# Kernel optimization log

Measured on AMD Instinct MI355X. Metric: run time of the kernel, lower is better.

The kernel has to match this reference:

```python
import jax, jax.numpy as jnp
import numpy as np

B, S, H = 1, 2048, 2048
E, I = 16, 1408
I_SHARED = 5632
TOP_K = 2


def setup_inputs() -> dict:
    key = jax.random.key(0)
    ks = jax.random.split(key, 8)
    scale = 0.02
    return {
        "hidden_states": jax.random.normal(ks[0], (B, S, H), dtype=jnp.float32),
        "router_w": jax.random.normal(ks[1], (H, E), dtype=jnp.float32) * scale,
        "expert_gate_up_w": jax.random.normal(ks[2], (E, H, 2 * I), dtype=jnp.float32) * scale,
        "expert_out_w": jax.random.normal(ks[3], (E, I, H), dtype=jnp.float32) * scale,
        "shared_ffw_gate_w": jax.random.normal(ks[4], (H, I_SHARED), dtype=jnp.float32) * scale,
        "shared_ffw_inter_w": jax.random.normal(ks[5], (H, I_SHARED), dtype=jnp.float32) * scale,
        "shared_ffw_out_w": jax.random.normal(ks[6], (I_SHARED, H), dtype=jnp.float32) * scale,
        "shared_gate_w": jax.random.normal(ks[7], (H, 1), dtype=jnp.float32) * scale,
        "top_k": TOP_K,
    }


def reference(hidden_states, router_w, expert_gate_up_w, expert_out_w,
              shared_ffw_gate_w, shared_ffw_inter_w, shared_ffw_out_w,
              shared_gate_w, top_k):
    b, s, h = hidden_states.shape
    e = router_w.shape[-1]
    x = hidden_states.reshape(-1, h)  # [T, H]

    # --- Router: softmax over experts, top-k, renormalize (norm_top_k_prob=True) ---
    router_logits = x @ router_w                        # [T, E]
    router_probs = jax.nn.softmax(router_logits, -1)
    top_p, top_i = jax.lax.top_k(router_probs, top_k)   # [T, K]
    top_p = top_p / jnp.sum(top_p, axis=-1, keepdims=True)
    # dense routing matrix [E, T] (matches one_hot-sum-transpose in source)
    one_hot = jax.nn.one_hot(top_i, e, dtype=top_p.dtype)  # [T, K, E]
    routing_full = jnp.sum(one_hot * top_p[..., None], axis=1).T  # [E, T]

    # --- Dense per-expert SwiGLU over ALL tokens (as in QwenMoeExperts) ---
    gate_up = jnp.einsum('th,ehm->etm', x, expert_gate_up_w)  # [E, T, 2I]
    gate, up = jnp.split(gate_up, 2, axis=-1)
    hidden = up * jax.nn.silu(gate)                           # [E, T, I]
    expert_out = jnp.einsum('eti,eih->eth', hidden, expert_out_w)  # [E, T, H]
    expert_contribution = jnp.einsum('eth,et->th', expert_out, routing_full)

    # --- Shared expert (SwiGLU MLP) with sigmoid gate ---
    sgate = jax.nn.silu(x @ shared_ffw_gate_w)
    sinter = x @ shared_ffw_inter_w
    shared_out = (sinter * sgate) @ shared_ffw_out_w          # [T, H]
    shared_out = shared_out * jax.nn.sigmoid(x @ shared_gate_w)

    out = (expert_contribution + shared_out).reshape(b, s, h)
    return out, router_logits
```

## Files before the change

kernel.cpp:

```cpp
#include <hip/hip_runtime.h>
#include <math.h>

typedef __attribute__((ext_vector_type(4))) float f32x4;
typedef __attribute__((ext_vector_type(2))) unsigned int u32x2;
typedef __attribute__((ext_vector_type(4))) unsigned int u32x4;
typedef __attribute__((ext_vector_type(8))) unsigned short u16x8;
typedef __attribute__((ext_vector_type(8))) __bf16 bf16x8;
typedef unsigned short ushort_t;

#define H_DIM 2048
#define T_TOK 2048
#define NEXP 16
#define I_DIM 1408
#define I2_DIM 2816
#define IS_DIM 5632
#define MAXROWS 6144

static __device__ __forceinline__ unsigned short f2bf(float f){
  union { float f; unsigned u; } v; v.f = f;
  unsigned r = v.u + 0x7FFFu + ((v.u >> 16) & 1u);
  return (unsigned short)(r >> 16);
}
static __device__ __forceinline__ float bf2f(unsigned short h){
  union { unsigned u; float f; } v; v.u = ((unsigned)h) << 16;
  return v.f;
}
static __device__ __forceinline__ float silu_f(float x){ return x / (1.f + __expf(-x)); }

static __device__ __forceinline__ void gld16(const ushort_t* g, ushort_t* l){
  __builtin_amdgcn_global_load_lds(
      (const __attribute__((address_space(1))) unsigned int*)g,
      (__attribute__((address_space(3))) unsigned int*)l, 16, 0, 0);
}

static __device__ __forceinline__ bf16x8 dsr128(unsigned byte_off){
  u32x4 r;
  asm volatile("ds_read_b128 %0, %1" : "=v"(r) : "v"(byte_off));
  return __builtin_bit_cast(bf16x8, r);
}

static __device__ __forceinline__ void tr_tile(const float* __restrict__ in,
                                               ushort_t* __restrict__ out,
                                               int K, int N, int k0, int n0){
  __shared__ float tl[128][65];
  int t = threadIdx.x;
  int lr = t >> 4;
  int lc = t & 15;
  #pragma unroll
  for (int p = 0; p < 8; p++){
    int row = p * 16 + lr;
    f32x4 v = *(const f32x4*)&in[(long)(k0 + row) * N + n0 + lc * 4];
    tl[row][lc*4 + 0] = v[0]; tl[row][lc*4 + 1] = v[1];
    tl[row][lc*4 + 2] = v[2]; tl[row][lc*4 + 3] = v[3];
  }
  __syncthreads();
  #pragma unroll
  for (int p = 0; p < 4; p++){
    int n = p * 16 + lr;
    int kc = lc * 8;
    union { ushort_t s[8]; u32x4 v; } pk;
    #pragma unroll
    for (int j = 0; j < 8; j++) pk.s[j] = f2bf(tl[kc + j][n]);
    *(u32x4*)&out[(long)(n0 + n) * K + k0 + kc] = pk.v;
  }
}

#define TR_O1 11264
#define TR_O2 16896
#define TR_O3 18304
#define TR_O4 19712
#define TR_TOT 21120

__global__ void transpose_all_k(const float* __restrict__ wgu, const float* __restrict__ wout,
                                const float* __restrict__ wsg, const float* __restrict__ wsi,
                                const float* __restrict__ wso,
                                ushort_t* __restrict__ wgu_t, ushort_t* __restrict__ wout_t,
                                ushort_t* __restrict__ wsg_t, ushort_t* __restrict__ wsi_t,
                                ushort_t* __restrict__ wso_t){
  int b = blockIdx.x;
  if (b < TR_O1){
    int e = b / 704, r = b % 704;
    int ky = r / 44, nx = r % 44;
    long zo = (long)e * H_DIM * I2_DIM;
    tr_tile(wgu + zo, wgu_t + zo, H_DIM, I2_DIM, ky * 128, nx * 64);
  } else if (b < TR_O2){
    int r = b - TR_O1;
    int e = r / 352; r %= 352;
    int ky = r / 32, nx = r % 32;
    long zo = (long)e * I_DIM * H_DIM;
    tr_tile(wout + zo, wout_t + zo, I_DIM, H_DIM, ky * 128, nx * 64);
  } else if (b < TR_O3){
    int r = b - TR_O2;
    int ky = r / 88, nx = r % 88;
    tr_tile(wsg, wsg_t, H_DIM, IS_DIM, ky * 128, nx * 64);
  } else if (b < TR_O4){
    int r = b - TR_O3;
    int ky = r / 88, nx = r % 88;
    tr_tile(wsi, wsi_t, H_DIM, IS_DIM, ky * 128, nx * 64);
  } else {
    int r = b - TR_O4;
    int ky = r / 32, nx = r % 32;
    tr_tile(wso, wso_t, IS_DIM, H_DIM, ky * 128, nx * 64);
  }
}

__global__ void router_k(const float* __restrict__ x, const float* __restrict__ rw,
                         const float* __restrict__ sgw, float* __restrict__ logits,
                         int* __restrict__ counts, int* __restrict__ lists,
                         float* __restrict__ probs, float* __restrict__ sgmul,
                         ushort_t* __restrict__ xb){
  int wid = threadIdx.x >> 6, lane = threadIdx.x & 63;
  int t = blockIdx.x * 4 + wid;
  const float* xr = x + (long)t * H_DIM;
  ushort_t* xbr = xb + (long)t * H_DIM;
  float acc[17];
  #pragma unroll
  for (int e = 0; e < 17; e++) acc[e] = 0.f;
  for (int h0 = lane * 4; h0 < H_DIM; h0 += 256){
    f32x4 xv = *(const f32x4*)&xr[h0];
    u32x2 pk;
    pk[0] = (unsigned)f2bf(xv[0]) | ((unsigned)f2bf(xv[1]) << 16);
    pk[1] = (unsigned)f2bf(xv[2]) | ((unsigned)f2bf(xv[3]) << 16);
    *(u32x2*)&xbr[h0] = pk;
    #pragma unroll
    for (int i = 0; i < 4; i++){
      float xs = xv[i];
      const float* wrow = rw + (long)(h0 + i) * NEXP;
      #pragma unroll
      for (int e = 0; e < 16; e++) acc[e] += xs * wrow[e];
      acc[16] += xs * sgw[h0 + i];
    }
  }
  #pragma unroll
  for (int e = 0; e < 17; e++)
    for (int off = 32; off >= 1; off >>= 1)
      acc[e] += __shfl_xor(acc[e], off);
  if (lane == 0){
    float* lo = logits + (long)t * NEXP;
    #pragma unroll
    for (int e = 0; e < 16; e++) lo[e] = acc[e];
    int e0 = 0;
    #pragma unroll
    for (int e = 1; e < 16; e++) if (acc[e] > acc[e0]) e0 = e;
    int e1 = (e0 == 0) ? 1 : 0;
    #pragma unroll
    for (int e = 0; e < 16; e++) if (e != e0 && acc[e] > acc[e1]) e1 = e;
    float d = acc[e1] - acc[e0];
    float ed = __expf(d);
    float p0 = 1.f / (1.f + ed);
    float p1 = ed / (1.f + ed);
    int pos0 = atomicAdd(&counts[e0], 1);
    lists[e0 * T_TOK + pos0] = t; probs[e0 * T_TOK + pos0] = p0;
    int pos1 = atomicAdd(&counts[e1], 1);
    lists[e1 * T_TOK + pos1] = t; probs[e1 * T_TOK + pos1] = p1;
    sgmul[t] = 1.f / (1.f + __expf(-acc[16]));
  }
}

__global__ void bases_k(const int* __restrict__ counts, int* __restrict__ bases){
  if (threadIdx.x == 0){
    int r = 0;
    for (int e = 0; e < NEXP; e++){ bases[e] = r; r += (counts[e] + 127) & ~127; }
  }
}

__global__ void swiglu_expert_k(const ushort_t* __restrict__ gu, ushort_t* __restrict__ hid){
  long qd = (long)blockIdx.x * 256 + threadIdx.x;
  long r = qd / (I_DIM / 8); int ic = (int)(qd % (I_DIM / 8)) * 8;
  const ushort_t* g = gu + r * I2_DIM + ic;
  u16x8 gv = *(const u16x8*)g;
  u16x8 uv = *(const u16x8*)(g + I_DIM);
  u16x8 ov;
  #pragma unroll
  for (int i = 0; i < 8; i++)
    ov[i] = f2bf(bf2f(uv[i]) * silu_f(bf2f(gv[i])));
  *(u16x8*)&hid[r * I_DIM + ic] = ov;
}

__global__ void swiglu_flat_k(ushort_t* __restrict__ sg, const ushort_t* __restrict__ si){
  long i = ((long)blockIdx.x * 256 + threadIdx.x) * 8;
  u16x8 g = *(const u16x8*)&sg[i];
  u16x8 s = *(const u16x8*)&si[i];
  u16x8 o;
  #pragma unroll
  for (int j = 0; j < 8; j++)
    o[j] = f2bf(bf2f(s[j]) * silu_f(bf2f(g[j])));
  *(u16x8*)&sg[i] = o;
}

template<int MODE>
static __device__ __forceinline__ void gemm3_body(
    const ushort_t* __restrict__ A, const ushort_t* __restrict__ Bt,
    const ushort_t* __restrict__ Bt2, ushort_t* __restrict__ Cb,
    int K, int lda, int ldbt, int ldc, int mb,
    const int* __restrict__ counts, const int* __restrict__ bases,
    const int* __restrict__ lists, const float* __restrict__ probs,
    const float* __restrict__ svec, float* __restrict__ outp, long bstride){
  int z = blockIdx.z;
  int cnt = T_TOK;
  const ushort_t* Ab = A;
  const ushort_t* Bb = Bt;
  long rbase = 0;
  if constexpr (MODE == 0){ if (z){ Bb = Bt2; Cb += (long)T_TOK * ldc; } }
  if constexpr (MODE == 1){ cnt = counts[z]; rbase = bases[z]; Bb += (long)z * bstride; }
  if constexpr (MODE == 2){ cnt = counts[z]; Ab += (long)bases[z] * lda; Bb += (long)z * bstride; }

  int kb = K / gridDim.y;
  int kbase = blockIdx.y * kb;
  Ab += kbase;
  Bb += kbase;

  int nwg = gridDim.x;
  int wgo = blockIdx.x;
  int q = nwg >> 3, r = nwg & 7;
  int xcd = wgo & 7, idx = wgo >> 3;
  int wg = (xcd < r ? xcd * (q + 1) : r * (q + 1) + (xcd - r) * q) + idx;
  int m0 = (wg % mb) * 128;
  if (m0 >= cnt) return;
  int n0 = (wg / mb) * 128;

  __shared__ ushort_t lds[3 * 8192];
  unsigned lbase = (unsigned)(size_t)(__attribute__((address_space(3))) ushort_t*)lds;

  int tid = threadIdx.x;
  int lane = tid & 63;
  int wv = tid >> 6;
  int wm = wv >> 1;
  int wn = wv & 1;

  int srow = lane >> 2;
  int sslot = ((lane & 3) ^ (srow & 3)) * 8;
  long aoff[2], boff[2];
  #pragma unroll
  for (int c = 0; c < 2; c++){
    int mr = wv * 32 + c * 16 + srow;
    int grow;
    if constexpr (MODE == 1){
      int j = m0 + mr; if (j >= cnt) j = cnt - 1;
      grow = lists[z * T_TOK + j];
    } else {
      grow = m0 + mr;
    }
    aoff[c] = (long)grow * lda + sslot;
    boff[c] = (long)(n0 + mr) * ldbt + sslot;
  }

  auto stage = [&](int t, int buf){
    long ko = (long)t * 32;
    ushort_t* dA = lds + buf * 8192 + wv * 1024;
    ushort_t* dB = dA + 4096;
    gld16(Ab + aoff[0] + ko, dA);
    gld16(Ab + aoff[1] + ko, dA + 512);
    gld16(Bb + boff[0] + ko, dB);
    gld16(Bb + boff[1] + ko, dB + 512);
  };

  f32x4 zero = {0.f, 0.f, 0.f, 0.f};
  f32x4 acc[4][4];
  #pragma unroll
  for (int i = 0; i < 4; i++)
    #pragma unroll
    for (int j = 0; j < 4; j++) acc[i][j] = zero;

  int fr = lane & 15;
  int kg = lane >> 4;
  unsigned ps = (unsigned)((kg ^ (fr & 3)) << 4);
  unsigned aoffb = (unsigned)((wm * 64 + fr) * 64) + ps;
  unsigned boffb = 8192u + (unsigned)((wn * 64 + fr) * 64) + ps;

  int nt = kb >> 5;
  stage(0, 0);
  __builtin_amdgcn_sched_barrier(0);
  stage(1, 1);

  int rb = 0, sb = 2;
  for (int t = 0; t < nt; t++){
    if (t + 2 < nt) asm volatile("s_waitcnt vmcnt(4)" ::: "memory");
    else            asm volatile("s_waitcnt vmcnt(0)" ::: "memory");
    __builtin_amdgcn_s_barrier();
    __builtin_amdgcn_sched_barrier(0);
    unsigned bufb = lbase + (unsigned)rb * 16384u;
    bf16x8 af[4], bg[4];
    #pragma unroll
    for (int f = 0; f < 4; f++){
      af[f] = dsr128(bufb + aoffb + f * 1024u);
      bg[f] = dsr128(bufb + boffb + f * 1024u);
    }
    __builtin_amdgcn_sched_barrier(0);
    if (t + 2 < nt) stage(t + 2, sb);
    asm volatile("s_waitcnt lgkmcnt(0)" ::: "memory");
    __builtin_amdgcn_sched_barrier(0);
    #pragma unroll
    for (int fm = 0; fm < 4; fm++)
      #pragma unroll
      for (int fn = 0; fn < 4; fn++)
        acc[fm][fn] = __builtin_amdgcn_mfma_f32_16x16x32_bf16(af[fm], bg[fn], acc[fm][fn], 0, 0, 0);
    rb = (rb == 2) ? 0 : rb + 1;
    sb = (sb == 2) ? 0 : sb + 1;
  }

  int colb = n0 + wn * 64 + (lane & 15);
  int rowb = m0 + wm * 64 + (lane >> 4) * 4;
  #pragma unroll
  for (int fm = 0; fm < 4; fm++){
    #pragma unroll
    for (int fn = 0; fn < 4; fn++){
      f32x4 v = acc[fm][fn];
      int col = colb + fn * 16;
      #pragma unroll
      for (int rr = 0; rr < 4; rr++){
        int m = rowb + fm * 16 + rr;
        if constexpr (MODE == 0){
          Cb[(long)m * ldc + col] = f2bf(v[rr]);
        } else if constexpr (MODE == 1){
          if (m < cnt) Cb[(rbase + m) * (long)ldc + col] = f2bf(v[rr]);
        } else if constexpr (MODE == 2){
          if (m < cnt){
            int tok = lists[z * T_TOK + m];
            float pp = probs[z * T_TOK + m];
            atomicAdd(outp + (long)tok * ldc + col, pp * v[rr]);
          }
        } else {
          atomicAdd(outp + (long)m * ldc + col, svec[m] * v[rr]);
        }
      }
    }
  }
}

#define GEMM_ARGS const ushort_t* A, const ushort_t* Bt, const ushort_t* Bt2, ushort_t* Cb, \
    int K, int lda, int ldbt, int ldc, int mb, const int* counts, const int* bases, \
    const int* lists, const float* probs, const float* svec, float* outp, long bstride
#define GEMM_PASS A, Bt, Bt2, Cb, K, lda, ldbt, ldc, mb, counts, bases, lists, probs, svec, outp, bstride

__global__ __launch_bounds__(256) void g_shared_gi(GEMM_ARGS){ gemm3_body<0>(GEMM_PASS); }
__global__ __launch_bounds__(256) void g_shared_out(GEMM_ARGS){ gemm3_body<3>(GEMM_PASS); }
__global__ __launch_bounds__(256) void g_expert_gu(GEMM_ARGS){ gemm3_body<1>(GEMM_PASS); }
__global__ __launch_bounds__(256) void g_expert_out(GEMM_ARGS){ gemm3_body<2>(GEMM_PASS); }

extern "C" void kernel_launch(void* const* d_in, const int* in_sizes, int n_in,
                              void* d_out, int out_size, void* d_ws, size_t ws_size,
                              hipStream_t stream){
  const float* x    = (const float*)d_in[0];
  const float* rw   = (const float*)d_in[1];
  const float* wgu  = (const float*)d_in[2];
  const float* wout = (const float*)d_in[3];
  const float* wsg  = (const float*)d_in[4];
  const float* wsi  = (const float*)d_in[5];
  const float* wso  = (const float*)d_in[6];
  const float* sgw  = (const float*)d_in[7];

  float* out = (float*)d_out;
  float* logits = out + (size_t)T_TOK * H_DIM;

  char* w = (char*)d_ws;
  auto alloc = [&](size_t b){ char* p = w; w += (b + 255) & ~(size_t)255; return p; };
  ushort_t* xb     = (ushort_t*)alloc((size_t)T_TOK * H_DIM * 2);
  ushort_t* wgu_t  = (ushort_t*)alloc((size_t)NEXP * I2_DIM * H_DIM * 2);
  ushort_t* wout_t = (ushort_t*)alloc((size_t)NEXP * H_DIM * I_DIM * 2);
  ushort_t* wsg_t  = (ushort_t*)alloc((size_t)IS_DIM * H_DIM * 2);
  ushort_t* wsi_t  = (ushort_t*)alloc((size_t)IS_DIM * H_DIM * 2);
  ushort_t* wso_t  = (ushort_t*)alloc((size_t)H_DIM * IS_DIM * 2);
  ushort_t* sgr    = (ushort_t*)alloc((size_t)2 * T_TOK * IS_DIM * 2);
  ushort_t* sir    = sgr + (size_t)T_TOK * IS_DIM;
  ushort_t* gu     = (ushort_t*)alloc((size_t)MAXROWS * I2_DIM * 2);
  ushort_t* hid    = (ushort_t*)alloc((size_t)MAXROWS * I_DIM * 2);
  int*   counts = (int*)alloc(64);
  int*   bases  = (int*)alloc(64);
  int*   lists  = (int*)alloc((size_t)NEXP * T_TOK * 4);
  float* probs  = (float*)alloc((size_t)NEXP * T_TOK * 4);
  float* sgmul  = (float*)alloc((size_t)T_TOK * 4);

  hipMemsetAsync(counts, 0, 64, stream);
  hipMemsetAsync(out, 0, (size_t)T_TOK * H_DIM * sizeof(float), stream);

  transpose_all_k<<<TR_TOT, 256, 0, stream>>>(wgu, wout, wsg, wsi, wso,
                                              wgu_t, wout_t, wsg_t, wsi_t, wso_t);
  router_k<<<512, 256, 0, stream>>>(x, rw, sgw, logits, counts, lists, probs, sgmul, xb);
  bases_k<<<1, 64, 0, stream>>>(counts, bases);

  g_shared_gi<<<dim3((T_TOK/128) * (IS_DIM/128), 1, 2), 256, 0, stream>>>(
      xb, wsg_t, wsi_t, sgr, H_DIM, H_DIM, H_DIM, IS_DIM, T_TOK/128,
      nullptr, nullptr, nullptr, nullptr, nullptr, nullptr, 0);
  swiglu_flat_k<<<(T_TOK * (IS_DIM/8)) / 256, 256, 0, stream>>>(sgr, sir);
  g_shared_out<<<dim3((T_TOK/128) * (H_DIM/128), 4, 1), 256, 0, stream>>>(
      sgr, wso_t, nullptr, nullptr, IS_DIM, IS_DIM, IS_DIM, H_DIM, T_TOK/128,
      nullptr, nullptr, nullptr, nullptr, sgmul, out, 0);

  g_expert_gu<<<dim3((T_TOK/128) * (I2_DIM/128), 1, NEXP), 256, 0, stream>>>(
      xb, wgu_t, nullptr, gu, H_DIM, H_DIM, H_DIM, I2_DIM, T_TOK/128,
      counts, bases, lists, probs, nullptr, nullptr, (long)I2_DIM * H_DIM);
  swiglu_expert_k<<<((long)MAXROWS * (I_DIM/8)) / 256, 256, 0, stream>>>(gu, hid);
  g_expert_out<<<dim3((T_TOK/128) * (H_DIM/128), 1, NEXP), 256, 0, stream>>>(
      hid, wout_t, nullptr, nullptr, I_DIM, I_DIM, I_DIM, H_DIM, T_TOK/128,
      counts, bases, lists, probs, nullptr, out, (long)I_DIM * H_DIM);

  (void)in_sizes; (void)n_in; (void)out_size; (void)ws_size;
}
```

Measured before the change: 778.5 us.

## Merge independent stages into combined launches and use nontemporal weight transposes

Folds the router into the weight-transpose launch, and pairs independent stages into shared grids: expert gate/up GEMM with the shared SwiGLU, and shared-out GEMM with the expert SwiGLU. This cuts kernel launches and lets blocks from independent work fill the GPU together. The templated GEMM becomes a runtime-mode core, and the transpose now uses nontemporal loads and stores. Runtime mode branches may cost registers or code quality in the GEMM inner epilogue.

```diff
diff --git a/kernel.cpp b/kernel.cpp
--- a/kernel.cpp
+++ b/kernel.cpp
@@ -32,11 +32,16 @@
       (const __attribute__((address_space(1))) unsigned int*)g,
       (__attribute__((address_space(3))) unsigned int*)l, 16, 0, 0);
 }
-
 static __device__ __forceinline__ bf16x8 dsr128(unsigned byte_off){
   u32x4 r;
   asm volatile("ds_read_b128 %0, %1" : "=v"(r) : "v"(byte_off));
   return __builtin_bit_cast(bf16x8, r);
+}
+
+static __device__ __forceinline__ int swz_r(int nwg, int wgo){
+  int q = nwg >> 3, r = nwg & 7;
+  int xcd = wgo & 7, idx = wgo >> 3;
+  return (xcd < r ? xcd * (q + 1) : r * (q + 1) + (xcd - r) * q) + idx;
 }
 
 static __device__ __forceinline__ void tr_tile(const float* __restrict__ in,
@@ -49,7 +54,7 @@
   #pragma unroll
   for (int p = 0; p < 8; p++){
     int row = p * 16 + lr;
-    f32x4 v = *(const f32x4*)&in[(long)(k0 + row) * N + n0 + lc * 4];
+    f32x4 v = __builtin_nontemporal_load((const f32x4*)&in[(long)(k0 + row) * N + n0 + lc * 4]);
     tl[row][lc*4 + 0] = v[0]; tl[row][lc*4 + 1] = v[1];
     tl[row][lc*4 + 2] = v[2]; tl[row][lc*4 + 3] = v[3];
   }
@@ -61,7 +66,7 @@
     union { ushort_t s[8]; u32x4 v; } pk;
     #pragma unroll
     for (int j = 0; j < 8; j++) pk.s[j] = f2bf(tl[kc + j][n]);
-    *(u32x4*)&out[(long)(n0 + n) * K + k0 + kc] = pk.v;
+    __builtin_nontemporal_store(pk.v, (u32x4*)&out[(long)(n0 + n) * K + k0 + kc]);
   }
 }
 
@@ -71,89 +76,91 @@
 #define TR_O4 19712
 #define TR_TOT 21120
 
-__global__ void transpose_all_k(const float* __restrict__ wgu, const float* __restrict__ wout,
-                                const float* __restrict__ wsg, const float* __restrict__ wsi,
-                                const float* __restrict__ wso,
-                                ushort_t* __restrict__ wgu_t, ushort_t* __restrict__ wout_t,
-                                ushort_t* __restrict__ wsg_t, ushort_t* __restrict__ wsi_t,
-                                ushort_t* __restrict__ wso_t){
+__global__ void k_tr_router(const float* __restrict__ x, const float* __restrict__ rw,
+                            const float* __restrict__ sgw, float* __restrict__ logits,
+                            int* __restrict__ counts, int* __restrict__ lists,
+                            float* __restrict__ probs, float* __restrict__ sgmul,
+                            ushort_t* __restrict__ xb,
+                            const float* __restrict__ wgu, const float* __restrict__ wout,
+                            const float* __restrict__ wsg, const float* __restrict__ wsi,
+                            const float* __restrict__ wso,
+                            ushort_t* __restrict__ wgu_t, ushort_t* __restrict__ wout_t,
+                            ushort_t* __restrict__ wsg_t, ushort_t* __restrict__ wsi_t,
+                            ushort_t* __restrict__ wso_t){
   int b = blockIdx.x;
-  if (b < TR_O1){
-    int e = b / 704, r = b % 704;
+  if (b < 512){
+    int wid = threadIdx.x >> 6, lane = threadIdx.x & 63;
+    int t = b * 4 + wid;
+    const float* xr = x + (long)t * H_DIM;
+    ushort_t* xbr = xb + (long)t * H_DIM;
+    float acc[17];
+    #pragma unroll
+    for (int e = 0; e < 17; e++) acc[e] = 0.f;
+    for (int h0 = lane * 4; h0 < H_DIM; h0 += 256){
+      f32x4 xv = *(const f32x4*)&xr[h0];
+      u32x2 pk;
+      pk[0] = (unsigned)f2bf(xv[0]) | ((unsigned)f2bf(xv[1]) << 16);
+      pk[1] = (unsigned)f2bf(xv[2]) | ((unsigned)f2bf(xv[3]) << 16);
+      *(u32x2*)&xbr[h0] = pk;
+      #pragma unroll
+      for (int i = 0; i < 4; i++){
+        float xs = xv[i];
+        const float* wrow = rw + (long)(h0 + i) * NEXP;
+        #pragma unroll
+        for (int e = 0; e < 16; e++) acc[e] += xs * wrow[e];
+        acc[16] += xs * sgw[h0 + i];
+      }
+    }
+    #pragma unroll
+    for (int e = 0; e < 17; e++)
+      for (int off = 32; off >= 1; off >>= 1)
+        acc[e] += __shfl_xor(acc[e], off);
+    if (lane == 0){
+      float* lo = logits + (long)t * NEXP;
+      #pragma unroll
+      for (int e = 0; e < 16; e++) lo[e] = acc[e];
+      int e0 = 0;
+      #pragma unroll
+      for (int e = 1; e < 16; e++) if (acc[e] > acc[e0]) e0 = e;
+      int e1 = (e0 == 0) ? 1 : 0;
+      #pragma unroll
+      for (int e = 0; e < 16; e++) if (e != e0 && acc[e] > acc[e1]) e1 = e;
+      float d = acc[e1] - acc[e0];
+      float ed = __expf(d);
+      float p0 = 1.f / (1.f + ed);
+      float p1 = ed / (1.f + ed);
+      int pos0 = atomicAdd(&counts[e0], 1);
+      lists[e0 * T_TOK + pos0] = t; probs[e0 * T_TOK + pos0] = p0;
+      int pos1 = atomicAdd(&counts[e1], 1);
+      lists[e1 * T_TOK + pos1] = t; probs[e1 * T_TOK + pos1] = p1;
+      sgmul[t] = 1.f / (1.f + __expf(-acc[16]));
+    }
+    return;
+  }
+  int bb = b - 512;
+  if (bb < TR_O1){
+    int e = bb / 704, r = bb % 704;
     int ky = r / 44, nx = r % 44;
     long zo = (long)e * H_DIM * I2_DIM;
     tr_tile(wgu + zo, wgu_t + zo, H_DIM, I2_DIM, ky * 128, nx * 64);
-  } else if (b < TR_O2){
-    int r = b - TR_O1;
+  } else if (bb < TR_O2){
+    int r = bb - TR_O1;
     int e = r / 352; r %= 352;
     int ky = r / 32, nx = r % 32;
     long zo = (long)e * I_DIM * H_DIM;
     tr_tile(wout + zo, wout_t + zo, I_DIM, H_DIM, ky * 128, nx * 64);
-  } else if (b < TR_O3){
-    int r = b - TR_O2;
+  } else if (bb < TR_O3){
+    int r = bb - TR_O2;
     int ky = r / 88, nx = r % 88;
     tr_tile(wsg, wsg_t, H_DIM, IS_DIM, ky * 128, nx * 64);
-  } else if (b < TR_O4){
-    int r = b - TR_O3;
+  } else if (bb < TR_O4){
+    int r = bb - TR_O3;
     int ky = r / 88, nx = r % 88;
     tr_tile(wsi, wsi_t, H_DIM, IS_DIM, ky * 128, nx * 64);
   } else {
-    int r = b - TR_O4;
+    int r = bb - TR_O4;
     int ky = r / 32, nx = r % 32;
     tr_tile(wso, wso_t, IS_DIM, H_DIM, ky * 128, nx * 64);
-  }
-}
-
-__global__ void router_k(const float* __restrict__ x, const float* __restrict__ rw,
-                         const float* __restrict__ sgw, float* __restrict__ logits,
-                         int* __restrict__ counts, int* __restrict__ lists,
-                         float* __restrict__ probs, float* __restrict__ sgmul,
-                         ushort_t* __restrict__ xb){
-  int wid = threadIdx.x >> 6, lane = threadIdx.x & 63;
-  int t = blockIdx.x * 4 + wid;
-  const float* xr = x + (long)t * H_DIM;
-  ushort_t* xbr = xb + (long)t * H_DIM;
-  float acc[17];
-  #pragma unroll
-  for (int e = 0; e < 17; e++) acc[e] = 0.f;
-  for (int h0 = lane * 4; h0 < H_DIM; h0 += 256){
-    f32x4 xv = *(const f32x4*)&xr[h0];
-    u32x2 pk;
-    pk[0] = (unsigned)f2bf(xv[0]) | ((unsigned)f2bf(xv[1]) << 16);
-    pk[1] = (unsigned)f2bf(xv[2]) | ((unsigned)f2bf(xv[3]) << 16);
-    *(u32x2*)&xbr[h0] = pk;
-    #pragma unroll
-    for (int i = 0; i < 4; i++){
-      float xs = xv[i];
-      const float* wrow = rw + (long)(h0 + i) * NEXP;
-      #pragma unroll
-      for (int e = 0; e < 16; e++) acc[e] += xs * wrow[e];
-      acc[16] += xs * sgw[h0 + i];
-    }
-  }
-  #pragma unroll
-  for (int e = 0; e < 17; e++)
-    for (int off = 32; off >= 1; off >>= 1)
-      acc[e] += __shfl_xor(acc[e], off);
-  if (lane == 0){
-    float* lo = logits + (long)t * NEXP;
-    #pragma unroll
-    for (int e = 0; e < 16; e++) lo[e] = acc[e];
-    int e0 = 0;
-    #pragma unroll
-    for (int e = 1; e < 16; e++) if (acc[e] > acc[e0]) e0 = e;
-    int e1 = (e0 == 0) ? 1 : 0;
-    #pragma unroll
-    for (int e = 0; e < 16; e++) if (e != e0 && acc[e] > acc[e1]) e1 = e;
-    float d = acc[e1] - acc[e0];
-    float ed = __expf(d);
-    float p0 = 1.f / (1.f + ed);
-    float p1 = ed / (1.f + ed);
-    int pos0 = atomicAdd(&counts[e0], 1);
-    lists[e0 * T_TOK + pos0] = t; probs[e0 * T_TOK + pos0] = p0;
-    int pos1 = atomicAdd(&counts[e1], 1);
-    lists[e1 * T_TOK + pos1] = t; probs[e1 * T_TOK + pos1] = p1;
-    sgmul[t] = 1.f / (1.f + __expf(-acc[16]));
   }
 }
 
@@ -164,61 +171,13 @@
   }
 }
 
-__global__ void swiglu_expert_k(const ushort_t* __restrict__ gu, ushort_t* __restrict__ hid){
-  long qd = (long)blockIdx.x * 256 + threadIdx.x;
-  long r = qd / (I_DIM / 8); int ic = (int)(qd % (I_DIM / 8)) * 8;
-  const ushort_t* g = gu + r * I2_DIM + ic;
-  u16x8 gv = *(const u16x8*)g;
-  u16x8 uv = *(const u16x8*)(g + I_DIM);
-  u16x8 ov;
-  #pragma unroll
-  for (int i = 0; i < 8; i++)
-    ov[i] = f2bf(bf2f(uv[i]) * silu_f(bf2f(gv[i])));
-  *(u16x8*)&hid[r * I_DIM + ic] = ov;
-}
-
-__global__ void swiglu_flat_k(ushort_t* __restrict__ sg, const ushort_t* __restrict__ si){
-  long i = ((long)blockIdx.x * 256 + threadIdx.x) * 8;
-  u16x8 g = *(const u16x8*)&sg[i];
-  u16x8 s = *(const u16x8*)&si[i];
-  u16x8 o;
-  #pragma unroll
-  for (int j = 0; j < 8; j++)
-    o[j] = f2bf(bf2f(s[j]) * silu_f(bf2f(g[j])));
-  *(u16x8*)&sg[i] = o;
-}
-
-template<int MODE>
-static __device__ __forceinline__ void gemm3_body(
-    const ushort_t* __restrict__ A, const ushort_t* __restrict__ Bt,
-    const ushort_t* __restrict__ Bt2, ushort_t* __restrict__ Cb,
-    int K, int lda, int ldbt, int ldc, int mb,
-    const int* __restrict__ counts, const int* __restrict__ bases,
-    const int* __restrict__ lists, const float* __restrict__ probs,
-    const float* __restrict__ svec, float* __restrict__ outp, long bstride){
-  int z = blockIdx.z;
-  int cnt = T_TOK;
-  const ushort_t* Ab = A;
-  const ushort_t* Bb = Bt;
-  long rbase = 0;
-  if constexpr (MODE == 0){ if (z){ Bb = Bt2; Cb += (long)T_TOK * ldc; } }
-  if constexpr (MODE == 1){ cnt = counts[z]; rbase = bases[z]; Bb += (long)z * bstride; }
-  if constexpr (MODE == 2){ cnt = counts[z]; Ab += (long)bases[z] * lda; Bb += (long)z * bstride; }
-
-  int kb = K / gridDim.y;
-  int kbase = blockIdx.y * kb;
-  Ab += kbase;
-  Bb += kbase;
-
-  int nwg = gridDim.x;
-  int wgo = blockIdx.x;
-  int q = nwg >> 3, r = nwg & 7;
-  int xcd = wgo & 7, idx = wgo >> 3;
-  int wg = (xcd < r ? xcd * (q + 1) : r * (q + 1) + (xcd - r) * q) + idx;
-  int m0 = (wg % mb) * 128;
-  if (m0 >= cnt) return;
-  int n0 = (wg / mb) * 128;
-
+static __device__ __forceinline__ void gemm_core(
+    const ushort_t* __restrict__ Ab, int lda,
+    const ushort_t* __restrict__ Bb, int ldbt, int kb,
+    int m0, int n0, int cnt, const int* __restrict__ gather, int emode,
+    ushort_t* __restrict__ Cb, int ldc, long rbase,
+    const int* __restrict__ sclist, const float* __restrict__ scprob,
+    const float* __restrict__ svec, float* __restrict__ outp){
   __shared__ ushort_t lds[3 * 8192];
   unsigned lbase = (unsigned)(size_t)(__attribute__((address_space(3))) ushort_t*)lds;
 
@@ -235,9 +194,9 @@
   for (int c = 0; c < 2; c++){
     int mr = wv * 32 + c * 16 + srow;
     int grow;
-    if constexpr (MODE == 1){
+    if (gather){
       int j = m0 + mr; if (j >= cnt) j = cnt - 1;
-      grow = lists[z * T_TOK + j];
+      grow = gather[j];
     } else {
       grow = m0 + mr;
     }
@@ -310,15 +269,14 @@
       #pragma unroll
       for (int rr = 0; rr < 4; rr++){
         int m = rowb + fm * 16 + rr;
-        if constexpr (MODE == 0){
+        if (emode == 0){
           Cb[(long)m * ldc + col] = f2bf(v[rr]);
-        } else if constexpr (MODE == 1){
+        } else if (emode == 1){
           if (m < cnt) Cb[(rbase + m) * (long)ldc + col] = f2bf(v[rr]);
-        } else if constexpr (MODE == 2){
+        } else if (emode == 2){
           if (m < cnt){
-            int tok = lists[z * T_TOK + m];
-            float pp = probs[z * T_TOK + m];
-            atomicAdd(outp + (long)tok * ldc + col, pp * v[rr]);
+            int tok = sclist[m];
+            atomicAdd(outp + (long)tok * ldc + col, scprob[m] * v[rr]);
           }
         } else {
           atomicAdd(outp + (long)m * ldc + col, svec[m] * v[rr]);
@@ -328,15 +286,82 @@
   }
 }
 
-#define GEMM_ARGS const ushort_t* A, const ushort_t* Bt, const ushort_t* Bt2, ushort_t* Cb, \
-    int K, int lda, int ldbt, int ldc, int mb, const int* counts, const int* bases, \
-    const int* lists, const float* probs, const float* svec, float* outp, long bstride
-#define GEMM_PASS A, Bt, Bt2, Cb, K, lda, ldbt, ldc, mb, counts, bases, lists, probs, svec, outp, bstride
-
-__global__ __launch_bounds__(256) void g_shared_gi(GEMM_ARGS){ gemm3_body<0>(GEMM_PASS); }
-__global__ __launch_bounds__(256) void g_shared_out(GEMM_ARGS){ gemm3_body<3>(GEMM_PASS); }
-__global__ __launch_bounds__(256) void g_expert_gu(GEMM_ARGS){ gemm3_body<1>(GEMM_PASS); }
-__global__ __launch_bounds__(256) void g_expert_out(GEMM_ARGS){ gemm3_body<2>(GEMM_PASS); }
+__global__ __launch_bounds__(256) void g_shared_gi(
+    const ushort_t* xb, const ushort_t* wsg_t, const ushort_t* wsi_t, ushort_t* sgr){
+  int z = blockIdx.z;
+  int wg = swz_r(704, blockIdx.x);
+  int m0 = (wg % 16) * 128, n0 = (wg / 16) * 128;
+  gemm_core(xb, H_DIM, (z ? wsi_t : wsg_t), H_DIM, H_DIM, m0, n0, T_TOK,
+            nullptr, 0, sgr + (size_t)z * T_TOK * IS_DIM, IS_DIM, 0,
+            nullptr, nullptr, nullptr, nullptr);
+}
+
+__global__ __launch_bounds__(256) void k_gu_flat(
+    const ushort_t* xb, const ushort_t* wgu_t, ushort_t* gu,
+    const int* counts, const int* bases, const int* lists,
+    ushort_t* sg, const ushort_t* si){
+  int b = blockIdx.x;
+  if (b < 5632){
+    int e = b / 352, r = b % 352;
+    int wr = swz_r(352, r);
+    int m0 = (wr % 16) * 128, n0 = (wr / 16) * 128;
+    int cnt = counts[e];
+    if (m0 >= cnt) return;
+    gemm_core(xb, H_DIM, wgu_t + (size_t)e * I2_DIM * H_DIM, H_DIM, H_DIM,
+              m0, n0, cnt, lists + e * T_TOK, 1, gu, I2_DIM, bases[e],
+              nullptr, nullptr, nullptr, nullptr);
+  } else {
+    long i = ((long)(b - 5632) * 256 + threadIdx.x) * 8;
+    u16x8 g = *(const u16x8*)&sg[i];
+    u16x8 s = *(const u16x8*)&si[i];
+    u16x8 o;
+    #pragma unroll
+    for (int j = 0; j < 8; j++)
+      o[j] = f2bf(bf2f(s[j]) * silu_f(bf2f(g[j])));
+    *(u16x8*)&sg[i] = o;
+  }
+}
+
+__global__ __launch_bounds__(256) void k_so_se(
+    const ushort_t* sgr, const ushort_t* wso_t, const float* sgmul, float* out,
+    const ushort_t* gu, ushort_t* hid){
+  int b = blockIdx.x;
+  if (b < 1024){
+    int kq = b >> 8, r = b & 255;
+    int wr = swz_r(256, r);
+    int m0 = (wr % 16) * 128, n0 = (wr / 16) * 128;
+    gemm_core(sgr + kq * (IS_DIM/4), IS_DIM, wso_t + kq * (IS_DIM/4), IS_DIM, IS_DIM/4,
+              m0, n0, T_TOK, nullptr, 3, nullptr, H_DIM, 0,
+              nullptr, nullptr, sgmul, out);
+  } else {
+    long qd = (long)(b - 1024) * 256 + threadIdx.x;
+    long r = qd / (I_DIM / 8); int ic = (int)(qd % (I_DIM / 8)) * 8;
+    const ushort_t* g = gu + r * I2_DIM + ic;
+    u16x8 gv = *(const u16x8*)g;
+    u16x8 uv = *(const u16x8*)(g + I_DIM);
+    u16x8 ov;
+    #pragma unroll
+    for (int i = 0; i < 8; i++)
+      ov[i] = f2bf(bf2f(uv[i]) * silu_f(bf2f(gv[i])));
+    *(u16x8*)&hid[r * I_DIM + ic] = ov;
+  }
+}
+
+__global__ __launch_bounds__(256) void k_eo(
+    const ushort_t* hid, const ushort_t* wout_t,
+    const int* counts, const int* bases, const int* lists, const float* probs,
+    float* out){
+  int b = blockIdx.x;
+  int e = b >> 8, r = b & 255;
+  int wr = swz_r(256, r);
+  int m0 = (wr % 16) * 128, n0 = (wr / 16) * 128;
+  int cnt = counts[e];
+  if (m0 >= cnt) return;
+  gemm_core(hid + (size_t)bases[e] * I_DIM, I_DIM,
+            wout_t + (size_t)e * H_DIM * I_DIM, I_DIM, I_DIM,
+            m0, n0, cnt, nullptr, 2, nullptr, H_DIM, 0,
+            lists + e * T_TOK, probs + e * T_TOK, nullptr, out);
+}
 
 extern "C" void kernel_launch(void* const* d_in, const int* in_sizes, int n_in,
                               void* d_out, int out_size, void* d_ws, size_t ws_size,
@@ -374,26 +399,18 @@
   hipMemsetAsync(counts, 0, 64, stream);
   hipMemsetAsync(out, 0, (size_t)T_TOK * H_DIM * sizeof(float), stream);
 
-  transpose_all_k<<<TR_TOT, 256, 0, stream>>>(wgu, wout, wsg, wsi, wso,
-                                              wgu_t, wout_t, wsg_t, wsi_t, wso_t);
-  router_k<<<512, 256, 0, stream>>>(x, rw, sgw, logits, counts, lists, probs, sgmul, xb);
+  k_tr_router<<<512 + TR_TOT, 256, 0, stream>>>(
+      x, rw, sgw, logits, counts, lists, probs, sgmul, xb,
+      wgu, wout, wsg, wsi, wso, wgu_t, wout_t, wsg_t, wsi_t, wso_t);
   bases_k<<<1, 64, 0, stream>>>(counts, bases);
 
-  g_shared_gi<<<dim3((T_TOK/128) * (IS_DIM/128), 1, 2), 256, 0, stream>>>(
-      xb, wsg_t, wsi_t, sgr, H_DIM, H_DIM, H_DIM, IS_DIM, T_TOK/128,
-      nullptr, nullptr, nullptr, nullptr, nullptr, nullptr, 0);
-  swiglu_flat_k<<<(T_TOK * (IS_DIM/8)) / 256, 256, 0, stream>>>(sgr, sir);
-  g_shared_out<<<dim3((T_TOK/128) * (H_DIM/128), 4, 1), 256, 0, stream>>>(
-      sgr, wso_t, nullptr, nullptr, IS_DIM, IS_DIM, IS_DIM, H_DIM, T_TOK/128,
-      nullptr, nullptr, nullptr, nullptr, sgmul, out, 0);
-
-  g_expert_gu<<<dim3((T_TOK/128) * (I2_DIM/128), 1, NEXP), 256, 0, stream>>>(
-      xb, wgu_t, nullptr, gu, H_DIM, H_DIM, H_DIM, I2_DIM, T_TOK/128,
-      counts, bases, lists, probs, nullptr, nullptr, (long)I2_DIM * H_DIM);
-  swiglu_expert_k<<<((long)MAXROWS * (I_DIM/8)) / 256, 256, 0, stream>>>(gu, hid);
-  g_expert_out<<<dim3((T_TOK/128) * (H_DIM/128), 1, NEXP), 256, 0, stream>>>(
-      hid, wout_t, nullptr, nullptr, I_DIM, I_DIM, I_DIM, H_DIM, T_TOK/128,
-      counts, bases, lists, probs, nullptr, out, (long)I_DIM * H_DIM);
+  g_shared_gi<<<dim3(704, 1, 2), 256, 0, stream>>>(xb, wsg_t, wsi_t, sgr);
+
+  k_gu_flat<<<5632 + 5632, 256, 0, stream>>>(xb, wgu_t, gu, counts, bases, lists, sgr, sir);
+
+  k_so_se<<<1024 + 4224, 256, 0, stream>>>(sgr, wso_t, sgmul, out, gu, hid);
+
+  k_eo<<<NEXP * 256, 256, 0, stream>>>(hid, wout_t, counts, bases, lists, probs, out);
 
   (void)in_sizes; (void)n_in; (void)out_size; (void)ws_size;
 }
```

Result: faster. 735.1 us (-5.6%).
